# Performance work log

Hardware: AMD Instinct MI355X
Metric: run time of the kernel (lower is better)

## Reference

```python
import jax, jax.numpy as jnp
import numpy as np

N_NODES = 50000
N_EDGES = 800000
N_REL = 2
K_SEL = 4096


def _glorot(key, shape):
    fan = shape[-2] + shape[-1]
    lim = jnp.sqrt(6.0 / fan)
    return jax.random.uniform(key, shape, minval=-lim, maxval=lim, dtype=jnp.float32)


def setup_inputs() -> dict:
    key = jax.random.key(0)
    ks = jax.random.split(key, 12)
    x = jax.random.normal(ks[0], (N_NODES, 128), jnp.float32)
    edge_index = jax.random.randint(ks[1], (2, N_EDGES), 0, N_NODES)
    edge_type = jax.random.randint(ks[2], (N_EDGES,), 0, N_REL)
    idx = jax.random.randint(ks[3], (K_SEL,), 0, N_NODES)
    # RGATConv 0: in=128, out=128, heads=2, dim=1 -> concat width 256
    w0 = _glorot(ks[4], (N_REL, 128, 256))
    q0 = _glorot(ks[5], (256, 2))
    k0 = _glorot(ks[6], (256, 2))
    b0 = jnp.zeros((256,), jnp.float32)
    g0 = jnp.ones((256,), jnp.float32)
    be0 = jnp.zeros((256,), jnp.float32)
    # RGATConv 1: in=256, out=128, heads=1
    w1 = _glorot(ks[7], (N_REL, 256, 128))
    q1 = _glorot(ks[8], (128, 1))
    k1 = _glorot(ks[9], (128, 1))
    b1 = jnp.zeros((128,), jnp.float32)
    g1 = jnp.ones((128,), jnp.float32)
    be1 = jnp.zeros((128,), jnp.float32)
    wm = _glorot(ks[10], (128, 5))
    bm = jnp.zeros((5,), jnp.float32)
    return dict(x=x, edge_index=edge_index, edge_type=edge_type, idx=idx,
                w0=w0, q0=q0, k0=k0, b0=b0, g0=g0, be0=be0,
                w1=w1, q1=q1, k1=k1, b1=b1, g1=g1, be1=be1, wm=wm, bm=bm)


def _segment_softmax(a, index, num_segments):
    # PyG utils.softmax: per-target max-shifted exp, normalized with +1e-16
    m = jax.ops.segment_max(a, index, num_segments=num_segments)
    m = jnp.where(jnp.isfinite(m), m, 0.0)
    e = jnp.exp(a - m[index])
    s = jax.ops.segment_sum(e, index, num_segments=num_segments)
    return e / (s[index] + 1e-16)


def _rgat(x, W, q, k, b, src, dst, edge_type, heads, out_ch, n):
    # additive-self-attention, across-relation, dim=1, aggr='add' (PyG defaults)
    xw = jnp.einsum('ni,rio->rno', x, W)          # [R, N, H*O]
    out_i = xw[edge_type, dst]                    # [E, H*O] gathered per edge
    out_j = xw[edge_type, src]                    # [E, H*O]
    alpha = jax.nn.leaky_relu(out_i @ q + out_j @ k, 0.2)   # [E, H]
    alpha = _segment_softmax(alpha, dst, n)
    msg = (alpha[:, :, None] * out_j.reshape(-1, heads, out_ch)).reshape(-1, heads * out_ch)
    return jax.ops.segment_sum(msg, dst, num_segments=n) + b


def _bn(h, g, b):
    # training-mode BatchNorm over nodes (biased var, eps=1e-5)
    mu = jnp.mean(h, axis=0)
    var = jnp.var(h, axis=0)
    return g * (h - mu) * jax.lax.rsqrt(var + 1e-5) + b


def reference(x, edge_index, edge_type, idx, w0, q0, k0, b0, g0, be0,
              w1, q1, k1, b1, g1, be1, wm, bm):
    n = x.shape[0]
    src, dst = edge_index[0], edge_index[1]
    h = jax.nn.leaky_relu(_rgat(x, w0, q0, k0, b0, src, dst, edge_type, 2, 128, n), 0.01)
    h = _bn(h, g0, be0)
    h = jax.nn.leaky_relu(_rgat(h, w1, q1, k1, b1, src, dst, edge_type, 1, 128, n), 0.01)
    h = _bn(h, g1, be1)
    h = h[idx]                                   # index_select over nodes
    out = jax.nn.sigmoid(h @ wm + bm)
    return (h, out)
```

## Files before the change

### kernel.cpp

```cpp
#include <hip/hip_runtime.h>
#include <hip/hip_bf16.h>
#include <math.h>


#define WAVE 64

typedef short     s16x8 __attribute__((ext_vector_type(8)));
typedef ushort    u16x8 __attribute__((ext_vector_type(8)));
typedef float     f32x4 __attribute__((ext_vector_type(4)));
typedef _Float16  f16x8 __attribute__((ext_vector_type(8)));

__device__ inline ushort bf_rne(float x) {
  uint u = __float_as_uint(x);
  return (ushort)((u + 0x7FFFu + ((u >> 16) & 1u)) >> 16);
}
__device__ inline ushort bf_hi_resid(float x, float& resid) {
  uint u = __float_as_uint(x);
  uint r = (u + 0x7FFFu + ((u >> 16) & 1u)) & 0xFFFF0000u;
  resid = x - __uint_as_float(r);
  return (ushort)(r >> 16);
}
__device__ inline float bf2f(ushort h) {
  return __uint_as_float(((uint)h) << 16);
}

__global__ __launch_bounds__(256) void k_hist(const int* __restrict__ dst,
                                              int* __restrict__ deg, int E) {
  int e = blockIdx.x * blockDim.x + threadIdx.x;
  if (e < E) atomicAdd(&deg[dst[e]], 1);
}

__global__ __launch_bounds__(256) void k_scan_blk(const int* __restrict__ deg,
                                                  int* __restrict__ bsum, int n) {
  int i = blockIdx.x * 256 + threadIdx.x;
  int v = (i < n) ? deg[i] : 0;
#pragma unroll
  for (int o = 32; o; o >>= 1) v += __shfl_xor(v, o);
  __shared__ int ws[4];
  if ((threadIdx.x & 63) == 0) ws[threadIdx.x >> 6] = v;
  __syncthreads();
  if (threadIdx.x == 0) bsum[blockIdx.x] = ws[0] + ws[1] + ws[2] + ws[3];
}

__global__ __launch_bounds__(256) void k_scan_top(int* __restrict__ bsum, int nb,
                                                  int* __restrict__ rowptr_n,
                                                  int E) {
  __shared__ int sh[256];
  int t = threadIdx.x;
  int carry = 0;
  for (int base = 0; base < nb; base += 256) {
    int i = base + t;
    int v = (i < nb) ? bsum[i] : 0;
    sh[t] = v;
    __syncthreads();
    for (int o = 1; o < 256; o <<= 1) {
      int u = (t >= o) ? sh[t - o] : 0;
      __syncthreads();
      sh[t] += u;
      __syncthreads();
    }
    if (i < nb) bsum[i] = carry + sh[t] - v;
    int blockTotal = sh[255];
    __syncthreads();
    carry += blockTotal;
  }
  if (t == 0) *rowptr_n = E;
}

__global__ __launch_bounds__(256) void k_scan_fin(const int* __restrict__ deg,
                                                  const int* __restrict__ bsum,
                                                  int* __restrict__ rowptr,
                                                  int* __restrict__ cursor, int n) {
  int t = threadIdx.x;
  int i = blockIdx.x * 256 + t;
  int v = (i < n) ? deg[i] : 0;
  __shared__ int sh[256];
  sh[t] = v;
  __syncthreads();
  for (int o = 1; o < 256; o <<= 1) {
    int u = (t >= o) ? sh[t - o] : 0;
    __syncthreads();
    sh[t] += u;
    __syncthreads();
  }
  if (i < n) {
    int ex = bsum[blockIdx.x] + sh[t] - v;
    rowptr[i] = ex;
    cursor[i] = ex;
  }
}

__global__ __launch_bounds__(256) void k_scatter(const int* __restrict__ dst,
                                                 int* __restrict__ cursor,
                                                 int* __restrict__ csr, int E) {
  int e = blockIdx.x * blockDim.x + threadIdx.x;
  if (e < E) {
    int p = atomicAdd(&cursor[dst[e]], 1);
    csr[p] = e;
  }
}

__global__ __launch_bounds__(256) void k_convW(const float* __restrict__ w,
                                               ushort* __restrict__ thi,
                                               ushort* __restrict__ tlo,
                                               const float* __restrict__ scale,
                                               int R, int K, int N) {
  int i = blockIdx.x * blockDim.x + threadIdx.x;
  if (i >= R * K * N) return;
  int n  = i % N;
  int t  = i / N;
  int kk = t % K;
  int r  = t / K;
  float x = w[i];
  if (scale) x *= scale[kk];
  float resid;
  ushort h = bf_hi_resid(x, resid);
  size_t o = ((size_t)r * N + n) * K + kk;
  thi[o] = h;
  tlo[o] = bf_rne(resid);
}

__global__ __launch_bounds__(256) void k_biasW(const float* __restrict__ w,
                                               const float* __restrict__ shf,
                                               float* __restrict__ cbias,
                                               int R, int K, int N) {
  int wid  = (blockIdx.x * blockDim.x + threadIdx.x) >> 6;
  int lane = threadIdx.x & 63;
  if (wid >= R * N) return;
  int n = wid % N, r = wid / N;
  float s = 0.f;
  for (int k = lane; k < K; k += WAVE)
    s += shf[k] * w[((size_t)r * K + k) * N + n];
#pragma unroll
  for (int o = 32; o; o >>= 1) s += __shfl_xor(s, o);
  if (lane == 0) cbias[wid] = s;
}

template <bool A32>
__global__ __launch_bounds__(256) void k_gemm_mfma(
    const float* __restrict__ A, const ushort* __restrict__ Ahi,
    const ushort* __restrict__ Alo, const ushort* __restrict__ Bhi,
    const ushort* __restrict__ Blo, const float* __restrict__ cbias,
    _Float16* __restrict__ C, int M, int K, int N) {
  const int nwgx = gridDim.x, nwgy = gridDim.y;
  int nwg = nwgx * nwgy * gridDim.z;
  int lin = blockIdx.x + nwgx * (blockIdx.y + nwgy * blockIdx.z);
  int q = nwg >> 3, rmd = nwg & 7, xcd = lin & 7, pos = lin >> 3;
  int swz = (xcd < rmd) ? xcd * (q + 1) + pos
                        : rmd * (q + 1) + (xcd - rmd) * q + pos;
  const int bx = swz % nwgx;
  const int by = (swz / nwgx) % nwgy;
  const int bz = swz / (nwgx * nwgy);

  const int r  = bz;
  const int n0 = bx * 128;
  const int m0 = by * 128;
  __shared__ __align__(16) ushort Ah[128][40];
  __shared__ __align__(16) ushort Al[128][40];
  __shared__ __align__(16) ushort Bh[128][40];
  __shared__ __align__(16) ushort Bl[128][40];
  const int tid  = threadIdx.x;
  const int lane = tid & 63;
  const int wid  = tid >> 6;
  const int wr = wid >> 1, wc = wid & 1;
  const int lr = lane & 15;
  const int lk = (lane >> 4) * 8;
  const size_t bbase = (size_t)r * N * K;

  f32x4 acc[4][4];
#pragma unroll
  for (int i = 0; i < 4; ++i)
#pragma unroll
    for (int j = 0; j < 4; ++j) acc[i][j] = (f32x4){0.f, 0.f, 0.f, 0.f};

  for (int k0 = 0; k0 < K; k0 += 32) {
#pragma unroll
    for (int rep = 0; rep < 2; ++rep) {
      int idx = tid + rep * 256;
      int row = idx >> 2, piece = idx & 3;
      int gm = m0 + row;
      if constexpr (A32) {
        f32x4 v0 = (f32x4){0.f, 0.f, 0.f, 0.f}, v1 = v0;
        if (gm < M) {
          const float* ga = A + (size_t)gm * K + k0 + piece * 8;
          v0 = *(const f32x4*)ga;
          v1 = *(const f32x4*)(ga + 4);
        }
        u16x8 hv, lv;
        float resid;
#pragma unroll
        for (int e = 0; e < 4; ++e) {
          hv[e] = bf_hi_resid(v0[e], resid); lv[e] = bf_rne(resid);
          hv[e + 4] = bf_hi_resid(v1[e], resid); lv[e + 4] = bf_rne(resid);
        }
        *(u16x8*)&Ah[row][piece * 8] = hv;
        *(u16x8*)&Al[row][piece * 8] = lv;
      } else {
        s16x8 vh = (s16x8)0, vl = (s16x8)0;
        if (gm < M) {
          size_t ga = (size_t)gm * K + k0 + piece * 8;
          vh = *(const s16x8*)(Ahi + ga);
          vl = *(const s16x8*)(Alo + ga);
        }
        *(s16x8*)&Ah[row][piece * 8] = vh;
        *(s16x8*)&Al[row][piece * 8] = vl;
      }
    }
#pragma unroll
    for (int rep = 0; rep < 2; ++rep) {
      int idx = tid + rep * 256;
      int col = idx >> 2, piece = idx & 3;
      size_t ga = bbase + (size_t)(n0 + col) * K + k0 + piece * 8;
      *(s16x8*)&Bh[col][piece * 8] = *(const s16x8*)(Bhi + ga);
      *(s16x8*)&Bl[col][piece * 8] = *(const s16x8*)(Blo + ga);
    }
    __syncthreads();

    s16x8 ah[4], al[4], bh[4], bl[4];
#pragma unroll
    for (int f = 0; f < 4; ++f) {
      ah[f] = *(const s16x8*)&Ah[wr * 64 + f * 16 + lr][lk];
      al[f] = *(const s16x8*)&Al[wr * 64 + f * 16 + lr][lk];
      bh[f] = *(const s16x8*)&Bh[wc * 64 + f * 16 + lr][lk];
      bl[f] = *(const s16x8*)&Bl[wc * 64 + f * 16 + lr][lk];
    }
#pragma unroll
    for (int fi = 0; fi < 4; ++fi)
#pragma unroll
      for (int fj = 0; fj < 4; ++fj) {
        acc[fi][fj] = __builtin_amdgcn_mfma_f32_16x16x32_bf16(
            ah[fi], bh[fj], acc[fi][fj], 0, 0, 0);
        acc[fi][fj] = __builtin_amdgcn_mfma_f32_16x16x32_bf16(
            ah[fi], bl[fj], acc[fi][fj], 0, 0, 0);
        acc[fi][fj] = __builtin_amdgcn_mfma_f32_16x16x32_bf16(
            al[fi], bh[fj], acc[fi][fj], 0, 0, 0);
      }
    __syncthreads();
  }

  float bz4[4] = {0.f, 0.f, 0.f, 0.f};
  if (cbias) {
#pragma unroll
    for (int fj = 0; fj < 4; ++fj)
      bz4[fj] = cbias[r * N + n0 + wc * 64 + fj * 16 + lr];
  }
  _Float16* Cr = C + (size_t)r * M * N;
#pragma unroll
  for (int fi = 0; fi < 4; ++fi) {
#pragma unroll
    for (int v = 0; v < 4; ++v) {
      int row = m0 + wr * 64 + fi * 16 + (lane >> 4) * 4 + v;
      if (row < M) {
        size_t rb = (size_t)row * N + n0 + wc * 64 + lr;
#pragma unroll
        for (int fj = 0; fj < 4; ++fj)
          Cr[rb + fj * 16] = (_Float16)(acc[fi][fj][v] + bz4[fj]);
      }
    }
  }
}

template <int C, int H>
__global__ __launch_bounds__(256) void k_logits(const _Float16* __restrict__ xw,
                                                const float* __restrict__ qm,
                                                const float* __restrict__ km,
                                                float* __restrict__ ai,
                                                float* __restrict__ aj,
                                                int totalRows) {
  int g = blockIdx.x * blockDim.x + threadIdx.x;
  int row = g >> 2, q4 = g & 3;
  if (row >= totalRows) return;
  constexpr int QC = C / 4;
  const _Float16* rp = xw + (size_t)row * C + q4 * QC;
  float pq[H] = {}, pk[H] = {};
  for (int b = 0; b < QC; b += 8) {
    f16x8 v = *(const f16x8*)(rp + b);
#pragma unroll
    for (int e = 0; e < 8; ++e) {
      float f = (float)v[e];
      int c = q4 * QC + b + e;
#pragma unroll
      for (int h = 0; h < H; ++h) {
        pq[h] += f * qm[c * H + h];
        pk[h] += f * km[c * H + h];
      }
    }
  }
#pragma unroll
  for (int h = 0; h < H; ++h) {
    pq[h] += __shfl_xor(pq[h], 1); pq[h] += __shfl_xor(pq[h], 2);
    pk[h] += __shfl_xor(pk[h], 1); pk[h] += __shfl_xor(pk[h], 2);
  }
  if (q4 == 0) {
#pragma unroll
    for (int h = 0; h < H; ++h) {
      ai[(size_t)row * H + h] = pq[h];
      aj[(size_t)row * H + h] = pk[h];
    }
  }
}

template <int C, int H, bool SPLIT>
__global__ __launch_bounds__(256) void k_agg(const int* __restrict__ rowptr,
                                             const int* __restrict__ csr,
                                             const int* __restrict__ srcIdx,
                                             const int* __restrict__ etype,
                                             const float* __restrict__ ai,
                                             const float* __restrict__ aj,
                                             const _Float16* __restrict__ xw,
                                             const float* __restrict__ bias,
                                             float* __restrict__ out32,
                                             ushort* __restrict__ ohi,
                                             ushort* __restrict__ olo,
                                             int nNodes) {
  constexpr int LPE = C / 8;
  constexpr int EPW = WAVE / LPE;
  constexpr int OC  = C / H;
  int wid  = (blockIdx.x * blockDim.x + threadIdx.x) >> 6;
  int lane = threadIdx.x & 63;
  if (wid >= nNodes) return;
  const int node  = wid;
  const int start = rowptr[node];
  const int end   = rowptr[node + 1];
  const int deg   = end - start;

  float aiv[2][H];
#pragma unroll
  for (int rr = 0; rr < 2; ++rr)
#pragma unroll
    for (int h = 0; h < H; ++h)
      aiv[rr][h] = ai[((size_t)rr * nNodes + node) * H + h];

  if (deg <= WAVE) {
    int i = start + lane;
    bool valid = i < end;
    int e = valid ? csr[i] : 0;
    int s = valid ? srcIdx[e] : 0;
    int t = valid ? etype[e] : 0;
    float a[H], eh[H], m[H], ssum[H];
#pragma unroll
    for (int h = 0; h < H; ++h) {
      float v = aiv[t][h] + aj[((size_t)t * nNodes + s) * H + h];
      v = v > 0.f ? v : 0.2f * v;
      a[h] = valid ? v : -1e30f;
      m[h] = a[h];
    }
#pragma unroll
    for (int h = 0; h < H; ++h)
#pragma unroll
      for (int o = 32; o; o >>= 1) m[h] = fmaxf(m[h], __shfl_xor(m[h], o));
#pragma unroll
    for (int h = 0; h < H; ++h) {
      eh[h] = valid ? expf(a[h] - m[h]) : 0.f;
      ssum[h] = eh[h];
#pragma unroll
      for (int o = 32; o; o >>= 1) ssum[h] += __shfl_xor(ssum[h], o);
    }

    const int sub = lane / LPE;
    const int cl  = lane % LPE;
    const int c0  = cl * 8;
    const int myhead = c0 / OC;

    float acc[8] = {};
#pragma unroll 4
    for (int j = 0; j < deg; j += EPW) {
      int je = j + sub;
      int   sj = __shfl(s, je);
      int   tj = __shfl(t, je);
      float cc0 = __shfl(eh[0], je);
      float coef;
      if (H == 1) coef = cc0;
      else { float cc1 = __shfl(eh[H - 1], je); coef = myhead ? cc1 : cc0; }
      f16x8 rv = *(const f16x8*)(xw + ((size_t)tj * nNodes + sj) * C + c0);
#pragma unroll
      for (int v = 0; v < 8; ++v) acc[v] += coef * (float)rv[v];
    }
#pragma unroll
    for (int v = 0; v < 8; ++v) {
      if (EPW == 4) acc[v] += __shfl_xor(acc[v], 16);
      acc[v] += __shfl_xor(acc[v], 32);
    }
    float inv = 1.f / (ssum[myhead] + 1e-16f);
    if (sub == 0) {
      if constexpr (SPLIT) {
        u16x8 hv, lv;
#pragma unroll
        for (int v = 0; v < 8; ++v) {
          float xo = acc[v] * inv + bias[c0 + v];
          xo = xo > 0.f ? xo : 0.01f * xo;
          float resid;
          hv[v] = bf_hi_resid(xo, resid);
          lv[v] = bf_rne(resid);
        }
        *(u16x8*)&ohi[(size_t)node * C + c0] = hv;
        *(u16x8*)&olo[(size_t)node * C + c0] = lv;
      } else {
        float ov[8];
#pragma unroll
        for (int v = 0; v < 8; ++v) {
          float xo = acc[v] * inv + bias[c0 + v];
          ov[v] = xo > 0.f ? xo : 0.01f * xo;
        }
        *(float4*)&out32[(size_t)node * C + c0]     = *(float4*)&ov[0];
        *(float4*)&out32[(size_t)node * C + c0 + 4] = *(float4*)&ov[4];
      }
    }
  } else {
    constexpr int VEC = C / WAVE;
    const int myhead = (lane * VEC) / OC;
    float acc[VEC] = {};
    float ssum[H] = {};
    float m[H];
#pragma unroll
    for (int h = 0; h < H; ++h) m[h] = -1e30f;
    for (int i = start + lane; i < end; i += WAVE) {
      int e = csr[i];
      int s = srcIdx[e];
      int t = etype[e];
#pragma unroll
      for (int h = 0; h < H; ++h) {
        float v = aiv[t][h] + aj[((size_t)t * nNodes + s) * H + h];
        v = v > 0.f ? v : 0.2f * v;
        m[h] = fmaxf(m[h], v);
      }
    }
#pragma unroll
    for (int h = 0; h < H; ++h)
#pragma unroll
      for (int o = 32; o; o >>= 1) m[h] = fmaxf(m[h], __shfl_xor(m[h], o));
    for (int base = start; base < end; base += WAVE) {
      int i = base + lane;
      bool valid = i < end;
      int e = valid ? csr[i] : 0;
      int s = valid ? srcIdx[e] : 0;
      int t = valid ? etype[e] : 0;
      float eh[H];
#pragma unroll
      for (int h = 0; h < H; ++h) {
        float v = aiv[t][h] + aj[((size_t)t * nNodes + s) * H + h];
        v = v > 0.f ? v : 0.2f * v;
        eh[h] = valid ? expf(v - m[h]) : 0.f;
        ssum[h] += eh[h];
      }
      int cnt = end - base; if (cnt > WAVE) cnt = WAVE;
#pragma unroll 4
      for (int j = 0; j < cnt; ++j) {
        int   sj = __shfl(s, j);
        int   tj = __shfl(t, j);
        float cc0 = __shfl(eh[0], j);
        float coef;
        if (H == 1) coef = cc0;
        else { float cc1 = __shfl(eh[H - 1], j); coef = myhead ? cc1 : cc0; }
        const _Float16* row = xw + ((size_t)tj * nNodes + sj) * C + lane * VEC;
#pragma unroll
        for (int v = 0; v < VEC; ++v) acc[v] += coef * (float)row[v];
      }
    }
#pragma unroll
    for (int h = 0; h < H; ++h)
#pragma unroll
      for (int o = 32; o; o >>= 1) ssum[h] += __shfl_xor(ssum[h], o);
    float inv = 1.f / (ssum[myhead] + 1e-16f);
#pragma unroll
    for (int v = 0; v < VEC; ++v) {
      int c = lane * VEC + v;
      float xo = acc[v] * inv + bias[c];
      xo = xo > 0.f ? xo : 0.01f * xo;
      if constexpr (SPLIT) {
        float resid;
        ohi[(size_t)node * C + c] = bf_hi_resid(xo, resid);
        olo[(size_t)node * C + c] = bf_rne(resid);
      } else {
        out32[(size_t)node * C + c] = xo;
      }
    }
  }
}

__global__ void k_bn_stats(const float* __restrict__ h, double* __restrict__ sum,
                           double* __restrict__ sumsq, int nNodes, int C) {
  int col = threadIdx.x;
  int r0 = blockIdx.x * 256;
  int r1 = r0 + 256; if (r1 > nNodes) r1 = nNodes;
  float s = 0.f, s2 = 0.f;
  for (int r = r0; r < r1; ++r) {
    float v = h[(size_t)r * C + col];
    s += v;
    s2 = fmaf(v, v, s2);
  }
  atomicAdd(&sum[col], (double)s);
  atomicAdd(&sumsq[col], (double)s2);
}

__global__ void k_bn_stats_hl(const ushort* __restrict__ hi,
                              const ushort* __restrict__ lo,
                              double* __restrict__ sum,
                              double* __restrict__ sumsq, int nNodes, int C) {
  int col = threadIdx.x;
  int r0 = blockIdx.x * 256;
  int r1 = r0 + 256; if (r1 > nNodes) r1 = nNodes;
  float s = 0.f, s2 = 0.f;
  for (int r = r0; r < r1; ++r) {
    size_t o = (size_t)r * C + col;
    float v = bf2f(hi[o]) + bf2f(lo[o]);
    s += v;
    s2 = fmaf(v, v, s2);
  }
  atomicAdd(&sum[col], (double)s);
  atomicAdd(&sumsq[col], (double)s2);
}

__global__ void k_bn_finalize(const double* __restrict__ sum,
                              const double* __restrict__ sumsq,
                              const float* __restrict__ g,
                              const float* __restrict__ be,
                              float* __restrict__ scale,
                              float* __restrict__ shift, int nNodes, int C) {
  int c = blockIdx.x * blockDim.x + threadIdx.x;
  if (c >= C) return;
  double mu  = sum[c] / nNodes;
  double var = sumsq[c] / nNodes - mu * mu;
  float rs = (float)(1.0 / sqrt(var + 1e-5));
  float sc = g[c] * rs;
  scale[c] = sc;
  shift[c] = be[c] - (float)mu * sc;
}

__global__ __launch_bounds__(256) void k_head(const float* __restrict__ h,
                                              const int* __restrict__ idx,
                                              const float* __restrict__ scl,
                                              const float* __restrict__ shf,
                                              const float* __restrict__ wm,
                                              const float* __restrict__ bm,
                                              float* __restrict__ outH,
                                              float* __restrict__ outP, int kSel) {
  int wid  = (blockIdx.x * blockDim.x + threadIdx.x) >> 6;
  int lane = threadIdx.x & 63;
  if (wid >= kSel) return;
  int node = idx[wid];
  const float* row = h + (size_t)node * 128;
  int c = lane * 2;
  float2 v = *(const float2*)&row[c];
  v.x = v.x * scl[c + 0] + shf[c + 0];
  v.y = v.y * scl[c + 1] + shf[c + 1];
  *(float2*)&outH[(size_t)wid * 128 + c] = v;
  float p0 = v.x * wm[c * 5 + 0] + v.y * wm[(c + 1) * 5 + 0];
  float p1 = v.x * wm[c * 5 + 1] + v.y * wm[(c + 1) * 5 + 1];
  float p2 = v.x * wm[c * 5 + 2] + v.y * wm[(c + 1) * 5 + 2];
  float p3 = v.x * wm[c * 5 + 3] + v.y * wm[(c + 1) * 5 + 3];
  float p4 = v.x * wm[c * 5 + 4] + v.y * wm[(c + 1) * 5 + 4];
#pragma unroll
  for (int o = 32; o; o >>= 1) {
    p0 += __shfl_xor(p0, o); p1 += __shfl_xor(p1, o); p2 += __shfl_xor(p2, o);
    p3 += __shfl_xor(p3, o); p4 += __shfl_xor(p4, o);
  }
  if (lane == 0) {
    float lg[5] = {p0 + bm[0], p1 + bm[1], p2 + bm[2], p3 + bm[3], p4 + bm[4]};
    float* o = &outP[(size_t)wid * 5];
    o[0] = 1.f / (1.f + expf(-lg[0]));
    o[1] = 1.f / (1.f + expf(-lg[1]));
    o[2] = 1.f / (1.f + expf(-lg[2]));
    o[3] = 1.f / (1.f + expf(-lg[3]));
    o[4] = 1.f / (1.f + expf(-lg[4]));
  }
}

extern "C" void kernel_launch(void* const* d_in, const int* in_sizes, int n_in,
                              void* d_out, int out_size, void* d_ws, size_t ws_size,
                              hipStream_t stream) {
  const float* x    = (const float*)d_in[0];
  const int*   ei   = (const int*)d_in[1];
  const int*   etyp = (const int*)d_in[2];
  const int*   idx  = (const int*)d_in[3];
  const float* w0   = (const float*)d_in[4];
  const float* q0   = (const float*)d_in[5];
  const float* k0   = (const float*)d_in[6];
  const float* b0   = (const float*)d_in[7];
  const float* g0   = (const float*)d_in[8];
  const float* be0  = (const float*)d_in[9];
  const float* w1   = (const float*)d_in[10];
  const float* q1   = (const float*)d_in[11];
  const float* k1   = (const float*)d_in[12];
  const float* b1   = (const float*)d_in[13];
  const float* g1   = (const float*)d_in[14];
  const float* be1  = (const float*)d_in[15];
  const float* wm   = (const float*)d_in[16];
  const float* bm   = (const float*)d_in[17];

  const int N    = in_sizes[0] / 128;
  const int E    = in_sizes[1] / 2;
  const int kSel = in_sizes[3];
  const int* srcIdx = ei;
  const int* dstIdx = ei + E;

  size_t off = 0;
  auto carve = [&](size_t bytes) -> void* {
    off = (off + 255) & ~(size_t)255;
    void* p = (char*)d_ws + off;
    off += bytes;
    return p;
  };
  int*      deg    = (int*)carve((size_t)N * 4);
  int*      rowptr = (int*)carve((size_t)(N + 1) * 4);
  int*      cursor = (int*)carve((size_t)N * 4);
  int*      bsum   = (int*)carve((size_t)((N + 255) / 256) * 4);
  int*      csr    = (int*)carve((size_t)E * 4);
  _Float16* xwh    = (_Float16*)carve((size_t)2 * N * 256 * 2);
  ushort*   Ahi    = (ushort*)carve((size_t)N * 256 * 2);
  ushort*   Alo    = (ushort*)carve((size_t)N * 256 * 2);
  ushort*   W0thi  = (ushort*)carve((size_t)2 * 256 * 128 * 2);
  ushort*   W0tlo  = (ushort*)carve((size_t)2 * 256 * 128 * 2);
  ushort*   W1thi  = (ushort*)carve((size_t)2 * 256 * 128 * 2);
  ushort*   W1tlo  = (ushort*)carve((size_t)2 * 256 * 128 * 2);
  float*    cbias1 = (float*)carve(256 * 4);
  float*    ai     = (float*)carve((size_t)2 * N * 2 * 4);
  float*    aj     = (float*)carve((size_t)2 * N * 2 * 4);
  float*    h1     = (float*)carve((size_t)N * 128 * 4);
  double*   dsum   = (double*)carve(256 * 8);
  double*   dsumsq = (double*)carve(256 * 8);
  float*    scl    = (float*)carve(256 * 4);
  float*    shf    = (float*)carve(256 * 4);

  float* outH = (float*)d_out;
  float* outP = outH + (size_t)kSel * 128;

  const int eb = (E + 255) / 256;
  const int nbBlocks = (N + 255) / 256;

  hipMemsetAsync(deg, 0, (size_t)N * 4, stream);
  k_hist<<<eb, 256, 0, stream>>>(dstIdx, deg, E);
  k_scan_blk<<<nbBlocks, 256, 0, stream>>>(deg, bsum, N);
  k_scan_top<<<1, 256, 0, stream>>>(bsum, nbBlocks, rowptr + N, E);
  k_scan_fin<<<nbBlocks, 256, 0, stream>>>(deg, bsum, rowptr, cursor, N);
  k_scatter<<<eb, 256, 0, stream>>>(dstIdx, cursor, csr, E);

  k_convW<<<(2 * 128 * 256 + 255) / 256, 256, 0, stream>>>(
      w0, W0thi, W0tlo, nullptr, 2, 128, 256);

  {
    dim3 grid(256 / 128, (N + 127) / 128, 2);
    k_gemm_mfma<true><<<grid, 256, 0, stream>>>(
        x, nullptr, nullptr, W0thi, W0tlo, nullptr, xwh, N, 128, 256);
  }
  k_logits<256, 2><<<(2 * N * 4 + 255) / 256, 256, 0, stream>>>(
      xwh, q0, k0, ai, aj, 2 * N);
  k_agg<256, 2, true><<<(N * WAVE + 255) / 256, 256, 0, stream>>>(
      rowptr, csr, srcIdx, etyp, ai, aj, xwh, b0, nullptr, Ahi, Alo, N);
  hipMemsetAsync(dsum, 0, 256 * 8, stream);
  hipMemsetAsync(dsumsq, 0, 256 * 8, stream);
  k_bn_stats_hl<<<nbBlocks, 256, 0, stream>>>(Ahi, Alo, dsum, dsumsq, N, 256);
  k_bn_finalize<<<1, 256, 0, stream>>>(dsum, dsumsq, g0, be0, scl, shf, N, 256);

  k_convW<<<(2 * 256 * 128 + 255) / 256, 256, 0, stream>>>(
      w1, W1thi, W1tlo, scl, 2, 256, 128);
  k_biasW<<<(2 * 128 * WAVE + 255) / 256, 256, 0, stream>>>(
      w1, shf, cbias1, 2, 256, 128);

  {
    dim3 grid(128 / 128, (N + 127) / 128, 2);
    k_gemm_mfma<false><<<grid, 256, 0, stream>>>(
        nullptr, Ahi, Alo, W1thi, W1tlo, cbias1, xwh, N, 256, 128);
  }
  k_logits<128, 1><<<(2 * N * 4 + 255) / 256, 256, 0, stream>>>(
      xwh, q1, k1, ai, aj, 2 * N);
  k_agg<128, 1, false><<<(N * WAVE + 255) / 256, 256, 0, stream>>>(
      rowptr, csr, srcIdx, etyp, ai, aj, xwh, b1, h1, nullptr, nullptr, N);
  hipMemsetAsync(dsum, 0, 128 * 8, stream);
  hipMemsetAsync(dsumsq, 0, 128 * 8, stream);
  k_bn_stats<<<nbBlocks, 128, 0, stream>>>(h1, dsum, dsumsq, N, 128);
  k_bn_finalize<<<1, 128, 0, stream>>>(dsum, dsumsq, g1, be1, scl, shf, N, 128);

  k_head<<<(kSel * WAVE + 255) / 256, 256, 0, stream>>>(
      h1, idx, scl, shf, wm, bm, outH, outP, kSel);
}
```

Baseline: 651.3 us.

## Fuse attention logit computation into MFMA GEMM epilogue with atomic accumulation

Drops the separate logits kernel and computes the per-row q/k dot products in the GEMM epilogue. Each wave reduces its 64-column slice with shuffles and atomically adds into zeroed ai/aj buffers. The block order is remapped so the relation index varies fastest, and memsets are merged on the assumption that ai/aj and dsum/dsumsq are contiguous. This avoids re-reading the fp16 xw output, at the cost of extra memsets, atomics and epilogue register pressure. Logits now come from pre-rounding fp32 values.

```diff
diff --git a/kernel.cpp b/kernel.cpp
--- a/kernel.cpp
+++ b/kernel.cpp
@@ -136,25 +136,26 @@
   if (lane == 0) cbias[wid] = s;
 }
 
-template <bool A32>
+template <bool A32, int H>
 __global__ __launch_bounds__(256) void k_gemm_mfma(
     const float* __restrict__ A, const ushort* __restrict__ Ahi,
     const ushort* __restrict__ Alo, const ushort* __restrict__ Bhi,
     const ushort* __restrict__ Blo, const float* __restrict__ cbias,
+    const float* __restrict__ qm, const float* __restrict__ km,
+    float* __restrict__ ai, float* __restrict__ aj,
     _Float16* __restrict__ C, int M, int K, int N) {
-  const int nwgx = gridDim.x, nwgy = gridDim.y;
-  int nwg = nwgx * nwgy * gridDim.z;
-  int lin = blockIdx.x + nwgx * (blockIdx.y + nwgy * blockIdx.z);
+  const int NX = gridDim.x, MY = gridDim.y, R = gridDim.z;
+  int nwg = NX * MY * R;
+  int lin = blockIdx.x + NX * (blockIdx.y + MY * blockIdx.z);
   int q = nwg >> 3, rmd = nwg & 7, xcd = lin & 7, pos = lin >> 3;
   int swz = (xcd < rmd) ? xcd * (q + 1) + pos
                         : rmd * (q + 1) + (xcd - rmd) * q + pos;
-  const int bx = swz % nwgx;
-  const int by = (swz / nwgx) % nwgy;
-  const int bz = swz / (nwgx * nwgy);
-
-  const int r  = bz;
-  const int n0 = bx * 128;
-  const int m0 = by * 128;
+  const int r  = swz % R;
+  const int nx = (swz / R) % NX;
+  const int my = swz / (R * NX);
+  const int n0 = nx * 128;
+  const int m0 = my * 128;
+
   __shared__ __align__(16) ushort Ah[128][40];
   __shared__ __align__(16) ushort Al[128][40];
   __shared__ __align__(16) ushort Bh[128][40];
@@ -244,58 +245,53 @@
     for (int fj = 0; fj < 4; ++fj)
       bz4[fj] = cbias[r * N + n0 + wc * 64 + fj * 16 + lr];
   }
+  float qv[4][H], kv[4][H];
+#pragma unroll
+  for (int fj = 0; fj < 4; ++fj) {
+    int gn = n0 + wc * 64 + fj * 16 + lr;
+#pragma unroll
+    for (int h = 0; h < H; ++h) {
+      qv[fj][h] = qm[gn * H + h];
+      kv[fj][h] = km[gn * H + h];
+    }
+  }
   _Float16* Cr = C + (size_t)r * M * N;
 #pragma unroll
   for (int fi = 0; fi < 4; ++fi) {
 #pragma unroll
     for (int v = 0; v < 4; ++v) {
       int row = m0 + wr * 64 + fi * 16 + (lane >> 4) * 4 + v;
+      float pq[H], pk[H];
+#pragma unroll
+      for (int h = 0; h < H; ++h) { pq[h] = 0.f; pk[h] = 0.f; }
       if (row < M) {
         size_t rb = (size_t)row * N + n0 + wc * 64 + lr;
 #pragma unroll
-        for (int fj = 0; fj < 4; ++fj)
-          Cr[rb + fj * 16] = (_Float16)(acc[fi][fj][v] + bz4[fj]);
-      }
-    }
-  }
-}
-
-template <int C, int H>
-__global__ __launch_bounds__(256) void k_logits(const _Float16* __restrict__ xw,
-                                                const float* __restrict__ qm,
-                                                const float* __restrict__ km,
-                                                float* __restrict__ ai,
-                                                float* __restrict__ aj,
-                                                int totalRows) {
-  int g = blockIdx.x * blockDim.x + threadIdx.x;
-  int row = g >> 2, q4 = g & 3;
-  if (row >= totalRows) return;
-  constexpr int QC = C / 4;
-  const _Float16* rp = xw + (size_t)row * C + q4 * QC;
-  float pq[H] = {}, pk[H] = {};
-  for (int b = 0; b < QC; b += 8) {
-    f16x8 v = *(const f16x8*)(rp + b);
-#pragma unroll
-    for (int e = 0; e < 8; ++e) {
-      float f = (float)v[e];
-      int c = q4 * QC + b + e;
+        for (int fj = 0; fj < 4; ++fj) {
+          float val = acc[fi][fj][v] + bz4[fj];
+          Cr[rb + fj * 16] = (_Float16)val;
+#pragma unroll
+          for (int h = 0; h < H; ++h) {
+            pq[h] += val * qv[fj][h];
+            pk[h] += val * kv[fj][h];
+          }
+        }
+      }
 #pragma unroll
       for (int h = 0; h < H; ++h) {
-        pq[h] += f * qm[c * H + h];
-        pk[h] += f * km[c * H + h];
-      }
-    }
-  }
-#pragma unroll
-  for (int h = 0; h < H; ++h) {
-    pq[h] += __shfl_xor(pq[h], 1); pq[h] += __shfl_xor(pq[h], 2);
-    pk[h] += __shfl_xor(pk[h], 1); pk[h] += __shfl_xor(pk[h], 2);
-  }
-  if (q4 == 0) {
-#pragma unroll
-    for (int h = 0; h < H; ++h) {
-      ai[(size_t)row * H + h] = pq[h];
-      aj[(size_t)row * H + h] = pk[h];
+#pragma unroll
+        for (int o = 1; o < 16; o <<= 1) {
+          pq[h] += __shfl_xor(pq[h], o);
+          pk[h] += __shfl_xor(pk[h], o);
+        }
+      }
+      if (lr == 0 && row < M) {
+#pragma unroll
+        for (int h = 0; h < H; ++h) {
+          atomicAdd(&ai[((size_t)r * M + row) * H + h], pq[h]);
+          atomicAdd(&aj[((size_t)r * M + row) * H + h], pk[h]);
+        }
+      }
     }
   }
 }
@@ -638,17 +634,16 @@
   k_convW<<<(2 * 128 * 256 + 255) / 256, 256, 0, stream>>>(
       w0, W0thi, W0tlo, nullptr, 2, 128, 256);
 
+  hipMemsetAsync(ai, 0, (size_t)2 * 2 * N * 2 * 4, stream);
   {
     dim3 grid(256 / 128, (N + 127) / 128, 2);
-    k_gemm_mfma<true><<<grid, 256, 0, stream>>>(
-        x, nullptr, nullptr, W0thi, W0tlo, nullptr, xwh, N, 128, 256);
-  }
-  k_logits<256, 2><<<(2 * N * 4 + 255) / 256, 256, 0, stream>>>(
-      xwh, q0, k0, ai, aj, 2 * N);
+    k_gemm_mfma<true, 2><<<grid, 256, 0, stream>>>(
+        x, nullptr, nullptr, W0thi, W0tlo, nullptr, q0, k0, ai, aj,
+        xwh, N, 128, 256);
+  }
   k_agg<256, 2, true><<<(N * WAVE + 255) / 256, 256, 0, stream>>>(
       rowptr, csr, srcIdx, etyp, ai, aj, xwh, b0, nullptr, Ahi, Alo, N);
-  hipMemsetAsync(dsum, 0, 256 * 8, stream);
-  hipMemsetAsync(dsumsq, 0, 256 * 8, stream);
+  hipMemsetAsync(dsum, 0, 2 * 256 * 8, stream);
   k_bn_stats_hl<<<nbBlocks, 256, 0, stream>>>(Ahi, Alo, dsum, dsumsq, N, 256);
   k_bn_finalize<<<1, 256, 0, stream>>>(dsum, dsumsq, g0, be0, scl, shf, N, 256);
 
@@ -657,17 +652,16 @@
   k_biasW<<<(2 * 128 * WAVE + 255) / 256, 256, 0, stream>>>(
       w1, shf, cbias1, 2, 256, 128);
 
+  hipMemsetAsync(ai, 0, (size_t)2 * 2 * N * 2 * 4, stream);
   {
     dim3 grid(128 / 128, (N + 127) / 128, 2);
-    k_gemm_mfma<false><<<grid, 256, 0, stream>>>(
-        nullptr, Ahi, Alo, W1thi, W1tlo, cbias1, xwh, N, 256, 128);
-  }
-  k_logits<128, 1><<<(2 * N * 4 + 255) / 256, 256, 0, stream>>>(
-      xwh, q1, k1, ai, aj, 2 * N);
+    k_gemm_mfma<false, 1><<<grid, 256, 0, stream>>>(
+        nullptr, Ahi, Alo, W1thi, W1tlo, cbias1, q1, k1, ai, aj,
+        xwh, N, 256, 128);
+  }
   k_agg<128, 1, false><<<(N * WAVE + 255) / 256, 256, 0, stream>>>(
       rowptr, csr, srcIdx, etyp, ai, aj, xwh, b1, h1, nullptr, nullptr, N);
-  hipMemsetAsync(dsum, 0, 128 * 8, stream);
-  hipMemsetAsync(dsumsq, 0, 128 * 8, stream);
+  hipMemsetAsync(dsum, 0, 2 * 256 * 8, stream);
   k_bn_stats<<<nbBlocks, 128, 0, stream>>>(h1, dsum, dsumsq, N, 128);
   k_bn_finalize<<<1, 128, 0, stream>>>(dsum, dsumsq, g1, be1, scl, shf, N, 128);
 
```

After: 637.4 us. 1.02x faster.
